# Kernel optimization log

Measured on AMD Instinct MI355X. Metric: run time of the kernel, lower is better.

## Reference

```python
import jax, jax.numpy as jnp
import numpy as np

INF = 1.0e15  # matches the TF module's 1e15 additive mask constant


def setup_inputs() -> dict:
    key = jax.random.key(0)
    kq, kk, kv, kp = jax.random.split(key, 4)
    B, S, D = 8, 4096, 64
    q = jax.random.normal(kq, (B, S, D), dtype=jnp.float32)
    k = jax.random.normal(kk, (B, S, D), dtype=jnp.float32)
    v = jax.random.normal(kv, (B, S, D), dtype=jnp.float32)
    # binary key-padding mask: 1 = masked. Broadcasts over seq_q.
    pad_mask = jax.random.randint(kp, (B, 1, S), 0, 2).astype(jnp.float32)
    # causal look-ahead mask: 1 above the diagonal (future positions masked)
    look_ahead_mask = (1.0 - jnp.tril(jnp.ones((S, S), dtype=jnp.float32)))
    return {"q": q, "k": k, "v": v, "pad_mask": pad_mask,
            "look_ahead_mask": look_ahead_mask}


def reference(q, k, v, pad_mask, look_ahead_mask):
    d_model = jnp.asarray(q.shape[2], dtype=q.dtype)
    # (B, Sq, Sk) score matrix, scaled
    score_logits = jnp.einsum("bqd,bkd->bqk", q, k) / jnp.sqrt(d_model)
    score_logits = score_logits + pad_mask * (-INF)          # broadcast (B,1,Sk)
    score_logits = score_logits + look_ahead_mask * (-INF)   # broadcast (Sq,Sk)
    attention_weight = jax.nn.softmax(score_logits, axis=-1)
    context_vector = jnp.einsum("bqk,bkd->bqd", attention_weight, v)
    return context_vector, attention_weight
```

## Files before the change

kernel.cpp:

```cpp
#include <hip/hip_runtime.h>

#define S_LEN 4096
#define D_DIM 64
#define NEG_BIG 1.0e15f
#define NC1 8
#define SSTAT (8 * 64 * NC1 * 64)
#define NPAD_OFF SSTAT
#define WS_FLOATS_NEEDED (NPAD_OFF + 16)
#define VSTRIDE 70

typedef __bf16 bf16_t;
typedef bf16_t bf16x8 __attribute__((ext_vector_type(8)));
typedef bf16_t bf16x4v __attribute__((ext_vector_type(4)));
typedef bf16_t bf16x2v __attribute__((ext_vector_type(2)));
typedef float f32x4v __attribute__((ext_vector_type(4)));

__global__ __launch_bounds__(256, 2)
void sdpa_stats(const float* __restrict__ Qg,
                const float* __restrict__ Kg,
                const float* __restrict__ Pg,
                float* __restrict__ ws,
                float* __restrict__ ctx)
{
    __shared__ __align__(16) bf16_t Ks[64][72];
    __shared__ float pads[64];

    const int tid  = threadIdx.x;
    const int w    = tid >> 6;
    const int lane = tid & 63;
    const int g    = lane >> 4;
    const int c    = lane & 15;
    const int gx   = blockIdx.x;
    const int b    = gx & 7;
    const int t    = gx >> 3;
    const int qt   = 63 - (t & 63);
    const int kc   = t >> 6;
    const int q0   = qt * 64;

    if (gx >= 2048) {
        f32x4v z = {0.f, 0.f, 0.f, 0.f};
        *(f32x4v*)(ctx + (size_t)(gx - 2048) * 1024 + tid * 4) = z;
    }

    const size_t soff = ((size_t)((b * 64 + qt) * NC1 + kc)) * 64;

    if (kc * 8 > qt) {
        if (tid < 64) ws[soff + tid] = 0.f;
        if (t == 511) {
            float cnt = 0.f, first = (float)S_LEN;
            const float* pb = Pg + (size_t)b * S_LEN;
            for (int i = tid; i < S_LEN; i += 256) {
                float p = pb[i];
                cnt += 1.f - p;
                if (p == 0.f) first = fminf(first, (float)i);
            }
            #pragma unroll
            for (int off = 32; off >= 1; off >>= 1) {
                cnt += __shfl_down(cnt, off);
                first = fminf(first, __shfl_down(first, off));
            }
            if (lane == 0) { pads[w] = cnt; pads[8 + w] = first; }
            __syncthreads();
            if (tid == 0) {
                ws[NPAD_OFF + b]     = pads[0] + pads[1] + pads[2] + pads[3];
                ws[NPAD_OFF + 8 + b] = fminf(fminf(pads[8], pads[9]), fminf(pads[10], pads[11]));
            }
        }
        return;
    }

    bf16x8 qa[2];
    {
        const float* qrow = Qg + ((size_t)b * S_LEN + q0 + 16 * w + c) * D_DIM;
        #pragma unroll
        for (int ks = 0; ks < 2; ++ks) {
            float4 a0 = *(const float4*)(qrow + ks * 32 + 8 * g);
            float4 a1 = *(const float4*)(qrow + ks * 32 + 8 * g + 4);
            qa[ks][0]=(bf16_t)a0.x; qa[ks][1]=(bf16_t)a0.y; qa[ks][2]=(bf16_t)a0.z; qa[ks][3]=(bf16_t)a0.w;
            qa[ks][4]=(bf16_t)a1.x; qa[ks][5]=(bf16_t)a1.y; qa[ks][6]=(bf16_t)a1.z; qa[ks][7]=(bf16_t)a1.w;
        }
    }

    float l[4] = {0.f, 0.f, 0.f, 0.f};
    const int qgBase = q0 + 16 * w + 4 * g;
    const int kend = min(kc * 8 + 8, qt + 1);

    for (int kt = kc * 8; kt < kend; ++kt) {
        const int k0 = kt * 64;
        {
            const float* src = Kg + ((size_t)b * S_LEN + k0) * D_DIM;
            #pragma unroll
            for (int i = 0; i < 4; ++i) {
                int f4 = i * 256 + tid;
                int r  = f4 >> 4;
                int c4 = (f4 & 15) * 4;
                float4 v4 = *(const float4*)(src + (size_t)f4 * 4);
                bf16x4v bv;
                bv[0]=(bf16_t)v4.x; bv[1]=(bf16_t)v4.y; bv[2]=(bf16_t)v4.z; bv[3]=(bf16_t)v4.w;
                *(bf16x4v*)&Ks[r][c4] = bv;
            }
            if (tid < 64) pads[tid] = Pg[(size_t)b * S_LEN + k0 + tid] * (-NEG_BIG);
        }
        __syncthreads();

        f32x4v sc[4];
        #pragma unroll
        for (int ct = 0; ct < 4; ++ct) {
            sc[ct] = (f32x4v){0.f, 0.f, 0.f, 0.f};
            #pragma unroll
            for (int ks = 0; ks < 2; ++ks) {
                bf16x8 kb = *(const bf16x8*)&Ks[ct * 16 + c][ks * 32 + 8 * g];
                sc[ct] = __builtin_amdgcn_mfma_f32_16x16x32_bf16(qa[ks], kb, sc[ct], 0, 0, 0);
            }
        }
        float rs[4] = {0.f, 0.f, 0.f, 0.f};
        #pragma unroll
        for (int ct = 0; ct < 4; ++ct) {
            float pn  = pads[ct * 16 + c];
            int   kgi = k0 + ct * 16 + c;
            #pragma unroll
            for (int r = 0; r < 4; ++r) {
                float lg = sc[ct][r] * 0.125f + pn;
                if (kgi > qgBase + r) lg -= NEG_BIG;
                rs[r] += __expf(lg);
            }
        }
        #pragma unroll
        for (int r = 0; r < 4; ++r) {
            float s = rs[r];
            s += __shfl_xor(s, 1);
            s += __shfl_xor(s, 2);
            s += __shfl_xor(s, 4);
            s += __shfl_xor(s, 8);
            l[r] += s;
        }
        __syncthreads();
    }

    if (c == 0) {
        #pragma unroll
        for (int r = 0; r < 4; ++r)
            ws[soff + 16 * w + 4 * g + r] = l[r];
    }
}

__global__ __launch_bounds__(256, 2)
void sdpa_wpv(const float* __restrict__ Qg,
              const float* __restrict__ Kg,
              const float* __restrict__ Vg,
              const float* __restrict__ Pg,
              float* __restrict__ Wg,
              float* __restrict__ ws,
              float* __restrict__ ctx)
{
    __shared__ __align__(16) bf16_t Ks[64][72];
    __shared__ __align__(16) bf16_t VT[64][VSTRIDE];
    __shared__ __align__(16) bf16_t Pf[64][72];
    __shared__ float pads[64];
    __shared__ float Lrow[64];

    const int tid  = threadIdx.x;
    const int w    = tid >> 6;
    const int lane = tid & 63;
    const int g    = lane >> 4;
    const int c    = lane & 15;
    const int gx   = blockIdx.x;
    const int b    = gx & 7;
    const int t    = gx >> 3;
    const int qt   = 63 - (t & 63);
    const int kc   = t >> 6;
    const int q0   = qt * 64;
    const int kstart = kc * 8;

    const float npadTot = ws[NPAD_OFF + b];
    const float firstNP = ws[NPAD_OFF + 8 + b];
    const bool  blockDeg = ((float)q0 < firstNP);

    if (tid < 64) {
        int qrow = q0 + tid;
        float L;
        if ((float)qrow < firstNP) {
            L = (float)(qrow + 1) + npadTot;
        } else {
            const float* sb = ws + (size_t)(b * 64 + qt) * NC1 * 64 + tid;
            L = 0.f;
            #pragma unroll
            for (int i = 0; i < NC1; ++i) L += sb[(size_t)i * 64];
        }
        Lrow[tid] = 1.f / L;
    }
    __syncthreads();

    float* wchunk = Wg + (size_t)b * S_LEN * S_LEN + (size_t)q0 * S_LEN;

    if (kstart > qt && !blockDeg) {
        const f32x4v z = {0.f, 0.f, 0.f, 0.f};
        for (int kt = kstart; kt < kstart + 8; ++kt) {
            float* wbase = wchunk + kt * 64;
            #pragma unroll
            for (int i = 0; i < 4; ++i) {
                int f4 = i * 256 + tid;
                int r  = f4 >> 4;
                int c4 = (f4 & 15) * 4;
                __builtin_nontemporal_store(z, (f32x4v*)(wbase + (size_t)r * S_LEN + c4));
            }
        }
        return;
    }

    bf16x8 qa[2];
    {
        const float* qrow = Qg + ((size_t)b * S_LEN + q0 + 16 * w + c) * D_DIM;
        #pragma unroll
        for (int ks = 0; ks < 2; ++ks) {
            float4 a0 = *(const float4*)(qrow + ks * 32 + 8 * g);
            float4 a1 = *(const float4*)(qrow + ks * 32 + 8 * g + 4);
            qa[ks][0]=(bf16_t)a0.x; qa[ks][1]=(bf16_t)a0.y; qa[ks][2]=(bf16_t)a0.z; qa[ks][3]=(bf16_t)a0.w;
            qa[ks][4]=(bf16_t)a1.x; qa[ks][5]=(bf16_t)a1.y; qa[ks][6]=(bf16_t)a1.z; qa[ks][7]=(bf16_t)a1.w;
        }
    }

    const int qgBase = q0 + 16 * w + 4 * g;
    float linv[4];
    #pragma unroll
    for (int r = 0; r < 4; ++r) linv[r] = Lrow[16 * w + 4 * g + r];

    f32x4v o[4];
    #pragma unroll
    for (int dt = 0; dt < 4; ++dt) o[dt] = (f32x4v){0.f, 0.f, 0.f, 0.f};

    for (int kt = kstart; kt < kstart + 8; ++kt) {
        const int k0 = kt * 64;
        float* wbase = wchunk + k0;
        const bool cur = (kt <= qt) || blockDeg;

        if (cur) {
            const float* ksrc = Kg + ((size_t)b * S_LEN + k0) * D_DIM;
            const float* vsrc = Vg + ((size_t)b * S_LEN + k0) * D_DIM;
            #pragma unroll
            for (int i = 0; i < 4; ++i) {
                int f4 = i * 256 + tid;
                int r  = f4 >> 4;
                int c4 = (f4 & 15) * 4;
                float4 kv = *(const float4*)(ksrc + (size_t)f4 * 4);
                bf16x4v bv;
                bv[0]=(bf16_t)kv.x; bv[1]=(bf16_t)kv.y; bv[2]=(bf16_t)kv.z; bv[3]=(bf16_t)kv.w;
                *(bf16x4v*)&Ks[r][c4] = bv;
                float4 vv = *(const float4*)(vsrc + (size_t)f4 * 4);
                VT[c4 + 0][r] = (bf16_t)vv.x;
                VT[c4 + 1][r] = (bf16_t)vv.y;
                VT[c4 + 2][r] = (bf16_t)vv.z;
                VT[c4 + 3][r] = (bf16_t)vv.w;
            }
            if (tid < 64) pads[tid] = Pg[(size_t)b * S_LEN + k0 + tid] * (-NEG_BIG);
            __syncthreads();

            f32x4v sc[4];
            #pragma unroll
            for (int ct = 0; ct < 4; ++ct) {
                sc[ct] = (f32x4v){0.f, 0.f, 0.f, 0.f};
                #pragma unroll
                for (int ks = 0; ks < 2; ++ks) {
                    bf16x8 kb = *(const bf16x8*)&Ks[ct * 16 + c][ks * 32 + 8 * g];
                    sc[ct] = __builtin_amdgcn_mfma_f32_16x16x32_bf16(qa[ks], kb, sc[ct], 0, 0, 0);
                }
            }
            if (!blockDeg) {
                #pragma unroll
                for (int ct = 0; ct < 4; ++ct) {
                    float pn  = pads[ct * 16 + c];
                    int   kgi = k0 + ct * 16 + c;
                    #pragma unroll
                    for (int r = 0; r < 4; ++r) {
                        float lg = sc[ct][r] * 0.125f + pn;
                        if (kgi > qgBase + r) lg -= NEG_BIG;
                        float wv = __expf(lg) * linv[r];
                        __builtin_nontemporal_store(wv,
                            wbase + (size_t)(16 * w + 4 * g + r) * S_LEN + ct * 16 + c);
                        Pf[16 * w + 4 * g + r][ct * 16 + c] = (bf16_t)wv;
                    }
                }
            } else {
                #pragma unroll
                for (int ct = 0; ct < 4; ++ct) {
                    float pn  = pads[ct * 16 + c];
                    int   kgi = k0 + ct * 16 + c;
                    #pragma unroll
                    for (int r = 0; r < 4; ++r) {
                        float lg = sc[ct][r] * 0.125f + pn;
                        if (kgi > qgBase + r) lg -= NEG_BIG;
                        float wv = __expf(lg) * linv[r];
                        if ((float)(qgBase + r) < firstNP)
                            wv = (kgi <= qgBase + r || pn == 0.f) ? linv[r] : 0.f;
                        __builtin_nontemporal_store(wv,
                            wbase + (size_t)(16 * w + 4 * g + r) * S_LEN + ct * 16 + c);
                        Pf[16 * w + 4 * g + r][ct * 16 + c] = (bf16_t)wv;
                    }
                }
            }
            __syncthreads();

            #pragma unroll
            for (int ks = 0; ks < 2; ++ks) {
                bf16x8 wa = *(const bf16x8*)&Pf[16 * w + c][ks * 32 + 8 * g];
                #pragma unroll
                for (int dt = 0; dt < 4; ++dt) {
                    bf16x8 vb;
                    #pragma unroll
                    for (int p = 0; p < 4; ++p)
                        ((bf16x2v*)&vb)[p] = *(const bf16x2v*)&VT[dt * 16 + c][ks * 32 + 8 * g + 2 * p];
                    o[dt] = __builtin_amdgcn_mfma_f32_16x16x32_bf16(wa, vb, o[dt], 0, 0, 0);
                }
            }
            __syncthreads();
        } else {
            const f32x4v z = {0.f, 0.f, 0.f, 0.f};
            #pragma unroll
            for (int i = 0; i < 4; ++i) {
                int f4 = i * 256 + tid;
                int r  = f4 >> 4;
                int c4 = (f4 & 15) * 4;
                __builtin_nontemporal_store(z, (f32x4v*)(wbase + (size_t)r * S_LEN + c4));
            }
        }
    }

    #pragma unroll
    for (int dt = 0; dt < 4; ++dt)
        #pragma unroll
        for (int r = 0; r < 4; ++r)
            atomicAdd(&ctx[((size_t)b * S_LEN + (q0 + 16 * w + 4 * g + r)) * D_DIM + dt * 16 + c],
                      o[dt][r]);
}

__global__ __launch_bounds__(256, 2)
void sdpa_fused(const float* __restrict__ Qg,
                const float* __restrict__ Kg,
                const float* __restrict__ Vg,
                const float* __restrict__ Pg,
                float* __restrict__ Og,
                float* __restrict__ Wg)
{
    __shared__ __align__(16) bf16_t Qs[64][72];
    __shared__ __align__(16) bf16_t Ks[64][72];
    __shared__ __align__(16) bf16_t VT[64][72];
    __shared__ __align__(16) float  Wf[64][68];
    __shared__ float pads[64];
    __shared__ float red[4];
    __shared__ int   anyDeg;

    const int tid  = threadIdx.x;
    const int w    = tid >> 6;
    const int lane = tid & 63;
    const int g    = lane >> 4;
    const int c    = lane & 15;
    const int b    = blockIdx.x & 7;
    const int qt   = 63 - (blockIdx.x >> 3);
    const int q0   = qt * 64;

    if (tid == 0) anyDeg = 0;

    {
        const float* src = Qg + ((size_t)b * S_LEN + q0) * D_DIM;
        #pragma unroll
        for (int i = 0; i < 4; ++i) {
            int f4 = i * 256 + tid;
            int r  = f4 >> 4;
            int c4 = (f4 & 15) * 4;
            float4 v4 = *(const float4*)(src + (size_t)f4 * 4);
            bf16x4v bv;
            bv[0]=(bf16_t)v4.x; bv[1]=(bf16_t)v4.y; bv[2]=(bf16_t)v4.z; bv[3]=(bf16_t)v4.w;
            *(bf16x4v*)&Qs[r][c4] = bv;
        }
    }
    __syncthreads();

    bf16x8 qa[2];
    {
        int row = 16 * w + c;
        #pragma unroll
        for (int ks = 0; ks < 2; ++ks)
            qa[ks] = *(const bf16x8*)&Qs[row][ks * 32 + 8 * g];
    }

    float m[4], l[4];
    #pragma unroll
    for (int r = 0; r < 4; ++r) { m[r] = -INFINITY; l[r] = 0.f; }
    const int qgBase = q0 + 16 * w + 4 * g;

    for (int kt = 0; kt <= qt; ++kt) {
        const int k0 = kt * 64;
        {
            const float* src = Kg + ((size_t)b * S_LEN + k0) * D_DIM;
            #pragma unroll
            for (int i = 0; i < 4; ++i) {
                int f4 = i * 256 + tid;
                int r  = f4 >> 4;
                int c4 = (f4 & 15) * 4;
                float4 v4 = *(const float4*)(src + (size_t)f4 * 4);
                bf16x4v bv;
                bv[0]=(bf16_t)v4.x; bv[1]=(bf16_t)v4.y; bv[2]=(bf16_t)v4.z; bv[3]=(bf16_t)v4.w;
                *(bf16x4v*)&Ks[r][c4] = bv;
            }
            if (tid < 64) pads[tid] = Pg[(size_t)b * S_LEN + k0 + tid] * (-NEG_BIG);
        }
        __syncthreads();

        f32x4v sc[4];
        #pragma unroll
        for (int ct = 0; ct < 4; ++ct) {
            sc[ct] = (f32x4v){0.f, 0.f, 0.f, 0.f};
            #pragma unroll
            for (int ks = 0; ks < 2; ++ks) {
                bf16x8 kb = *(const bf16x8*)&Ks[ct * 16 + c][ks * 32 + 8 * g];
                sc[ct] = __builtin_amdgcn_mfma_f32_16x16x32_bf16(qa[ks], kb, sc[ct], 0, 0, 0);
            }
        }
        float l4[4][4];
        #pragma unroll
        for (int ct = 0; ct < 4; ++ct) {
            float pn  = pads[ct * 16 + c];
            int   kgi = k0 + ct * 16 + c;
            #pragma unroll
            for (int r = 0; r < 4; ++r) {
                float lg = sc[ct][r] * 0.125f + pn;
                if (kgi > qgBase + r) lg -= NEG_BIG;
                l4[ct][r] = lg;
            }
        }
        #pragma unroll
        for (int r = 0; r < 4; ++r) {
            float tm = fmaxf(fmaxf(l4[0][r], l4[1][r]), fmaxf(l4[2][r], l4[3][r]));
            tm = fmaxf(tm, __shfl_xor(tm, 1));
            tm = fmaxf(tm, __shfl_xor(tm, 2));
            tm = fmaxf(tm, __shfl_xor(tm, 4));
            tm = fmaxf(tm, __shfl_xor(tm, 8));
            float mnew = fmaxf(m[r], tm);
            float s = __expf(l4[0][r] - mnew) + __expf(l4[1][r] - mnew)
                    + __expf(l4[2][r] - mnew) + __expf(l4[3][r] - mnew);
            s += __shfl_xor(s, 1);
            s += __shfl_xor(s, 2);
            s += __shfl_xor(s, 4);
            s += __shfl_xor(s, 8);
            l[r] = l[r] * __expf(m[r] - mnew) + s;
            m[r] = mnew;
        }
        __syncthreads();
    }

    {
        float cnt = 0.f;
        const float* pb = Pg + (size_t)b * S_LEN;
        for (int i = tid; i < S_LEN; i += 256) cnt += 1.f - pb[i];
        #pragma unroll
        for (int off = 32; off >= 1; off >>= 1) cnt += __shfl_down(cnt, off);
        if (lane == 0) red[w] = cnt;
    }
    __syncthreads();
    {
        float nonpad = red[0] + red[1] + red[2] + red[3];
        bool deg = false;
        #pragma unroll
        for (int r = 0; r < 4; ++r)
            if (m[r] < -1.0e14f) { l[r] += nonpad; deg = true; }
        if (deg) anyDeg = 1;
    }
    __syncthreads();
    const bool blockDeg = (anyDeg != 0);
    float linv[4];
    #pragma unroll
    for (int r = 0; r < 4; ++r) linv[r] = 1.f / l[r];

    f32x4v o[4];
    #pragma unroll
    for (int dt = 0; dt < 4; ++dt) o[dt] = (f32x4v){0.f, 0.f, 0.f, 0.f};

    for (int kt = 0; kt < 64; ++kt) {
        const int k0 = kt * 64;
        float* wbase = Wg + (size_t)b * S_LEN * S_LEN + (size_t)q0 * S_LEN + k0;

        if (kt <= qt || blockDeg) {
            const float* ksrc = Kg + ((size_t)b * S_LEN + k0) * D_DIM;
            const float* vsrc = Vg + ((size_t)b * S_LEN + k0) * D_DIM;
            #pragma unroll
            for (int i = 0; i < 4; ++i) {
                int f4 = i * 256 + tid;
                int r  = f4 >> 4;
                int c4 = (f4 & 15) * 4;
                float4 kv = *(const float4*)(ksrc + (size_t)f4 * 4);
                bf16x4v bv;
                bv[0]=(bf16_t)kv.x; bv[1]=(bf16_t)kv.y; bv[2]=(bf16_t)kv.z; bv[3]=(bf16_t)kv.w;
                *(bf16x4v*)&Ks[r][c4] = bv;
                float4 vv = *(const float4*)(vsrc + (size_t)f4 * 4);
                VT[c4 + 0][r] = (bf16_t)vv.x;
                VT[c4 + 1][r] = (bf16_t)vv.y;
                VT[c4 + 2][r] = (bf16_t)vv.z;
                VT[c4 + 3][r] = (bf16_t)vv.w;
            }
            if (tid < 64) pads[tid] = Pg[(size_t)b * S_LEN + k0 + tid] * (-NEG_BIG);
            __syncthreads();

            f32x4v sc[4];
            #pragma unroll
            for (int ct = 0; ct < 4; ++ct) {
                sc[ct] = (f32x4v){0.f, 0.f, 0.f, 0.f};
                #pragma unroll
                for (int ks = 0; ks < 2; ++ks) {
                    bf16x8 kb = *(const bf16x8*)&Ks[ct * 16 + c][ks * 32 + 8 * g];
                    sc[ct] = __builtin_amdgcn_mfma_f32_16x16x32_bf16(qa[ks], kb, sc[ct], 0, 0, 0);
                }
            }
            #pragma unroll
            for (int ct = 0; ct < 4; ++ct) {
                float pn  = pads[ct * 16 + c];
                int   kgi = k0 + ct * 16 + c;
                #pragma unroll
                for (int r = 0; r < 4; ++r) {
                    float lg = sc[ct][r] * 0.125f + pn;
                    if (kgi > qgBase + r) lg -= NEG_BIG;
                    float wv = __expf(lg - m[r]) * linv[r];
                    Wf[16 * w + 4 * g + r][ct * 16 + c] = wv;
                }
            }
            __syncthreads();

            #pragma unroll
            for (int i = 0; i < 4; ++i) {
                int f4 = i * 256 + tid;
                int r  = f4 >> 4;
                int c4 = (f4 & 15) * 4;
                float4 wv = *(const float4*)&Wf[r][c4];
                *(float4*)(wbase + (size_t)r * S_LEN + c4) = wv;
            }

            #pragma unroll
            for (int ks = 0; ks < 2; ++ks) {
                float4 f0 = *(const float4*)&Wf[16 * w + c][ks * 32 + 8 * g];
                float4 f1 = *(const float4*)&Wf[16 * w + c][ks * 32 + 8 * g + 4];
                bf16x8 wa;
                wa[0]=(bf16_t)f0.x; wa[1]=(bf16_t)f0.y; wa[2]=(bf16_t)f0.z; wa[3]=(bf16_t)f0.w;
                wa[4]=(bf16_t)f1.x; wa[5]=(bf16_t)f1.y; wa[6]=(bf16_t)f1.z; wa[7]=(bf16_t)f1.w;
                #pragma unroll
                for (int dt = 0; dt < 4; ++dt) {
                    bf16x8 vb = *(const bf16x8*)&VT[dt * 16 + c][ks * 32 + 8 * g];
                    o[dt] = __builtin_amdgcn_mfma_f32_16x16x32_bf16(wa, vb, o[dt], 0, 0, 0);
                }
            }
            __syncthreads();
        } else {
            const float4 z = {0.f, 0.f, 0.f, 0.f};
            #pragma unroll
            for (int i = 0; i < 4; ++i) {
                int f4 = i * 256 + tid;
                int r  = f4 >> 4;
                int c4 = (f4 & 15) * 4;
                *(float4*)(wbase + (size_t)r * S_LEN + c4) = z;
            }
        }
    }

    #pragma unroll
    for (int dt = 0; dt < 4; ++dt)
        #pragma unroll
        for (int r = 0; r < 4; ++r)
            Og[((size_t)b * S_LEN + (q0 + 16 * w + 4 * g + r)) * D_DIM + dt * 16 + c] = o[dt][r];
}

extern "C" void kernel_launch(void* const* d_in, const int* in_sizes, int n_in,
                              void* d_out, int out_size, void* d_ws, size_t ws_size,
                              hipStream_t stream) {
    const float* q   = (const float*)d_in[0];
    const float* k   = (const float*)d_in[1];
    const float* v   = (const float*)d_in[2];
    const float* pad = (const float*)d_in[3];

    float* out  = (float*)d_out;
    float* ctx  = out;
    float* attw = out + (size_t)8 * 4096 * 64;
    float* ws   = (float*)d_ws;

    if (ws_size >= (size_t)WS_FLOATS_NEEDED * 4) {
        hipLaunchKernelGGL(sdpa_stats, dim3(4096), dim3(256), 0, stream, q, k, pad, ws, ctx);
        hipLaunchKernelGGL(sdpa_wpv,   dim3(4096), dim3(256), 0, stream, q, k, v, pad, attw, ws, ctx);
    } else {
        hipLaunchKernelGGL(sdpa_fused, dim3(512), dim3(256), 0, stream, q, k, v, pad, ctx, attw);
    }
}
```

Measured before the change: 192.6 us.

## Merge stats and weight kernels into one ticket-ordered launch with flag dependencies

```diff
diff --git a/kernel.cpp b/kernel.cpp
--- a/kernel.cpp
+++ b/kernel.cpp
@@ -6,7 +6,9 @@
 #define NC1 8
 #define SSTAT (8 * 64 * NC1 * 64)
 #define NPAD_OFF SSTAT
-#define WS_FLOATS_NEEDED (NPAD_OFF + 16)
+#define FLAGS_OFF (NPAD_OFF + 16)
+#define TICKET_OFF (FLAGS_OFF + 512)
+#define WS_FLOATS_NEEDED (TICKET_OFF + 1)
 #define VSTRIDE 70
 
 typedef __bf16 bf16_t;
@@ -15,166 +17,200 @@
 typedef bf16_t bf16x2v __attribute__((ext_vector_type(2)));
 typedef float f32x4v __attribute__((ext_vector_type(4)));
 
+__global__ void sdpa_prep(const float* __restrict__ Pg, float* __restrict__ ws)
+{
+    __shared__ float red[16];
+    const int b   = blockIdx.x;
+    const int tid = threadIdx.x;
+    int* flags = (int*)(ws + FLAGS_OFF);
+    if (tid < 64) flags[b * 64 + tid] = 0;
+    if (b == 0 && tid == 128) ((int*)(ws + TICKET_OFF))[0] = 0;
+
+    float cnt = 0.f, first = (float)S_LEN;
+    const float* pb = Pg + (size_t)b * S_LEN;
+    for (int i = tid; i < S_LEN; i += 256) {
+        float p = pb[i];
+        cnt += 1.f - p;
+        if (p == 0.f) first = fminf(first, (float)i);
+    }
+    #pragma unroll
+    for (int off = 32; off >= 1; off >>= 1) {
+        cnt += __shfl_down(cnt, off);
+        first = fminf(first, __shfl_down(first, off));
+    }
+    const int w = tid >> 6, lane = tid & 63;
+    if (lane == 0) { red[w] = cnt; red[8 + w] = first; }
+    __syncthreads();
+    if (tid == 0) {
+        ws[NPAD_OFF + b]     = red[0] + red[1] + red[2] + red[3];
+        ws[NPAD_OFF + 8 + b] = fminf(fminf(red[8], red[9]), fminf(red[10], red[11]));
+    }
+}
+
 __global__ __launch_bounds__(256, 2)
-void sdpa_stats(const float* __restrict__ Qg,
-                const float* __restrict__ Kg,
-                const float* __restrict__ Pg,
-                float* __restrict__ ws,
-                float* __restrict__ ctx)
-{
-    __shared__ __align__(16) bf16_t Ks[64][72];
-    __shared__ float pads[64];
-
-    const int tid  = threadIdx.x;
-    const int w    = tid >> 6;
-    const int lane = tid & 63;
-    const int g    = lane >> 4;
-    const int c    = lane & 15;
-    const int gx   = blockIdx.x;
-    const int b    = gx & 7;
-    const int t    = gx >> 3;
-    const int qt   = 63 - (t & 63);
-    const int kc   = t >> 6;
-    const int q0   = qt * 64;
-
-    if (gx >= 2048) {
-        f32x4v z = {0.f, 0.f, 0.f, 0.f};
-        *(f32x4v*)(ctx + (size_t)(gx - 2048) * 1024 + tid * 4) = z;
-    }
-
-    const size_t soff = ((size_t)((b * 64 + qt) * NC1 + kc)) * 64;
-
-    if (kc * 8 > qt) {
-        if (tid < 64) ws[soff + tid] = 0.f;
-        if (t == 511) {
-            float cnt = 0.f, first = (float)S_LEN;
-            const float* pb = Pg + (size_t)b * S_LEN;
-            for (int i = tid; i < S_LEN; i += 256) {
-                float p = pb[i];
-                cnt += 1.f - p;
-                if (p == 0.f) first = fminf(first, (float)i);
-            }
-            #pragma unroll
-            for (int off = 32; off >= 1; off >>= 1) {
-                cnt += __shfl_down(cnt, off);
-                first = fminf(first, __shfl_down(first, off));
-            }
-            if (lane == 0) { pads[w] = cnt; pads[8 + w] = first; }
-            __syncthreads();
-            if (tid == 0) {
-                ws[NPAD_OFF + b]     = pads[0] + pads[1] + pads[2] + pads[3];
-                ws[NPAD_OFF + 8 + b] = fminf(fminf(pads[8], pads[9]), fminf(pads[10], pads[11]));
-            }
-        }
-        return;
-    }
-
-    bf16x8 qa[2];
-    {
-        const float* qrow = Qg + ((size_t)b * S_LEN + q0 + 16 * w + c) * D_DIM;
-        #pragma unroll
-        for (int ks = 0; ks < 2; ++ks) {
-            float4 a0 = *(const float4*)(qrow + ks * 32 + 8 * g);
-            float4 a1 = *(const float4*)(qrow + ks * 32 + 8 * g + 4);
-            qa[ks][0]=(bf16_t)a0.x; qa[ks][1]=(bf16_t)a0.y; qa[ks][2]=(bf16_t)a0.z; qa[ks][3]=(bf16_t)a0.w;
-            qa[ks][4]=(bf16_t)a1.x; qa[ks][5]=(bf16_t)a1.y; qa[ks][6]=(bf16_t)a1.z; qa[ks][7]=(bf16_t)a1.w;
-        }
-    }
-
-    float l[4] = {0.f, 0.f, 0.f, 0.f};
-    const int qgBase = q0 + 16 * w + 4 * g;
-    const int kend = min(kc * 8 + 8, qt + 1);
-
-    for (int kt = kc * 8; kt < kend; ++kt) {
-        const int k0 = kt * 64;
-        {
-            const float* src = Kg + ((size_t)b * S_LEN + k0) * D_DIM;
-            #pragma unroll
-            for (int i = 0; i < 4; ++i) {
-                int f4 = i * 256 + tid;
-                int r  = f4 >> 4;
-                int c4 = (f4 & 15) * 4;
-                float4 v4 = *(const float4*)(src + (size_t)f4 * 4);
-                bf16x4v bv;
-                bv[0]=(bf16_t)v4.x; bv[1]=(bf16_t)v4.y; bv[2]=(bf16_t)v4.z; bv[3]=(bf16_t)v4.w;
-                *(bf16x4v*)&Ks[r][c4] = bv;
-            }
-            if (tid < 64) pads[tid] = Pg[(size_t)b * S_LEN + k0 + tid] * (-NEG_BIG);
-        }
-        __syncthreads();
-
-        f32x4v sc[4];
-        #pragma unroll
-        for (int ct = 0; ct < 4; ++ct) {
-            sc[ct] = (f32x4v){0.f, 0.f, 0.f, 0.f};
-            #pragma unroll
-            for (int ks = 0; ks < 2; ++ks) {
-                bf16x8 kb = *(const bf16x8*)&Ks[ct * 16 + c][ks * 32 + 8 * g];
-                sc[ct] = __builtin_amdgcn_mfma_f32_16x16x32_bf16(qa[ks], kb, sc[ct], 0, 0, 0);
-            }
-        }
-        float rs[4] = {0.f, 0.f, 0.f, 0.f};
-        #pragma unroll
-        for (int ct = 0; ct < 4; ++ct) {
-            float pn  = pads[ct * 16 + c];
-            int   kgi = k0 + ct * 16 + c;
-            #pragma unroll
-            for (int r = 0; r < 4; ++r) {
-                float lg = sc[ct][r] * 0.125f + pn;
-                if (kgi > qgBase + r) lg -= NEG_BIG;
-                rs[r] += __expf(lg);
-            }
-        }
-        #pragma unroll
-        for (int r = 0; r < 4; ++r) {
-            float s = rs[r];
-            s += __shfl_xor(s, 1);
-            s += __shfl_xor(s, 2);
-            s += __shfl_xor(s, 4);
-            s += __shfl_xor(s, 8);
-            l[r] += s;
-        }
-        __syncthreads();
-    }
-
-    if (c == 0) {
-        #pragma unroll
-        for (int r = 0; r < 4; ++r)
-            ws[soff + 16 * w + 4 * g + r] = l[r];
-    }
-}
-
-__global__ __launch_bounds__(256, 2)
-void sdpa_wpv(const float* __restrict__ Qg,
-              const float* __restrict__ Kg,
-              const float* __restrict__ Vg,
-              const float* __restrict__ Pg,
-              float* __restrict__ Wg,
-              float* __restrict__ ws,
-              float* __restrict__ ctx)
+void sdpa_main(const float* __restrict__ Qg,
+               const float* __restrict__ Kg,
+               const float* __restrict__ Vg,
+               const float* __restrict__ Pg,
+               float* __restrict__ Wg,
+               float* __restrict__ ws,
+               float* __restrict__ ctx)
 {
     __shared__ __align__(16) bf16_t Ks[64][72];
     __shared__ __align__(16) bf16_t VT[64][VSTRIDE];
     __shared__ __align__(16) bf16_t Pf[64][72];
     __shared__ float pads[64];
     __shared__ float Lrow[64];
-
-    const int tid  = threadIdx.x;
+    __shared__ int   tkt;
+
+    const int tid = threadIdx.x;
+    int* flags = (int*)(ws + FLAGS_OFF);
+    if (tid == 0) tkt = atomicAdd((int*)(ws + TICKET_OFF), 1);
+    __syncthreads();
+    const int ticket = tkt;
+
     const int w    = tid >> 6;
     const int lane = tid & 63;
     const int g    = lane >> 4;
     const int c    = lane & 15;
-    const int gx   = blockIdx.x;
-    const int b    = gx & 7;
-    const int t    = gx >> 3;
-    const int qt   = 63 - (t & 63);
-    const int kc   = t >> 6;
-    const int q0   = qt * 64;
+
+    if (ticket < 4096) {
+        const int qt  = 63 - (ticket >> 6);
+        const int rem = ticket & 63;
+        const int kc  = rem >> 3;
+        const int b   = rem & 7;
+        const int q0  = qt * 64;
+        const int bqt = b * 64 + qt;
+
+        if (kc > (qt >> 3)) {
+            if (tid == 0) { __threadfence(); atomicAdd(flags + bqt, 1); }
+            return;
+        }
+
+        if (kc == 0) {
+            f32x4v z = {0.f, 0.f, 0.f, 0.f};
+            float* cb = ctx + ((size_t)b * S_LEN + q0) * D_DIM;
+            #pragma unroll
+            for (int i = 0; i < 4; ++i)
+                *(f32x4v*)(cb + i * 1024 + tid * 4) = z;
+        }
+
+        bf16x8 qa[2];
+        {
+            const float* qrow = Qg + ((size_t)b * S_LEN + q0 + 16 * w + c) * D_DIM;
+            #pragma unroll
+            for (int ks = 0; ks < 2; ++ks) {
+                float4 a0 = *(const float4*)(qrow + ks * 32 + 8 * g);
+                float4 a1 = *(const float4*)(qrow + ks * 32 + 8 * g + 4);
+                qa[ks][0]=(bf16_t)a0.x; qa[ks][1]=(bf16_t)a0.y; qa[ks][2]=(bf16_t)a0.z; qa[ks][3]=(bf16_t)a0.w;
+                qa[ks][4]=(bf16_t)a1.x; qa[ks][5]=(bf16_t)a1.y; qa[ks][6]=(bf16_t)a1.z; qa[ks][7]=(bf16_t)a1.w;
+            }
+        }
+
+        float l[4] = {0.f, 0.f, 0.f, 0.f};
+        const int qgBase = q0 + 16 * w + 4 * g;
+        const int kend = min(kc * 8 + 8, qt + 1);
+
+        for (int kt = kc * 8; kt < kend; ++kt) {
+            const int k0 = kt * 64;
+            {
+                const float* src = Kg + ((size_t)b * S_LEN + k0) * D_DIM;
+                #pragma unroll
+                for (int i = 0; i < 4; ++i) {
+                    int f4 = i * 256 + tid;
+                    int r  = f4 >> 4;
+                    int c4 = (f4 & 15) * 4;
+                    float4 v4 = *(const float4*)(src + (size_t)f4 * 4);
+                    bf16x4v bv;
+                    bv[0]=(bf16_t)v4.x; bv[1]=(bf16_t)v4.y; bv[2]=(bf16_t)v4.z; bv[3]=(bf16_t)v4.w;
+                    *(bf16x4v*)&Ks[r][c4] = bv;
+                }
+                if (tid < 64) pads[tid] = Pg[(size_t)b * S_LEN + k0 + tid] * (-NEG_BIG);
+            }
+            __syncthreads();
+
+            f32x4v sc[4];
+            #pragma unroll
+            for (int ct = 0; ct < 4; ++ct) {
+                sc[ct] = (f32x4v){0.f, 0.f, 0.f, 0.f};
+                #pragma unroll
+                for (int ks = 0; ks < 2; ++ks) {
+                    bf16x8 kb = *(const bf16x8*)&Ks[ct * 16 + c][ks * 32 + 8 * g];
+                    sc[ct] = __builtin_amdgcn_mfma_f32_16x16x32_bf16(qa[ks], kb, sc[ct], 0, 0, 0);
+                }
+            }
+            float rs[4] = {0.f, 0.f, 0.f, 0.f};
+            #pragma unroll
+            for (int ct = 0; ct < 4; ++ct) {
+                float pn  = pads[ct * 16 + c];
+                int   kgi = k0 + ct * 16 + c;
+                #pragma unroll
+                for (int r = 0; r < 4; ++r) {
+                    float lg = sc[ct][r] * 0.125f + pn;
+                    if (kgi > qgBase + r) lg -= NEG_BIG;
+                    rs[r] += __expf(lg);
+                }
+            }
+            #pragma unroll
+            for (int r = 0; r < 4; ++r) {
+                float s = rs[r];
+                s += __shfl_xor(s, 1);
+                s += __shfl_xor(s, 2);
+                s += __shfl_xor(s, 4);
+                s += __shfl_xor(s, 8);
+                l[r] += s;
+            }
+            __syncthreads();
+        }
+
+        const size_t soff = ((size_t)(bqt * NC1 + kc)) * 64;
+        if (c == 0) {
+            #pragma unroll
+            for (int r = 0; r < 4; ++r)
+                ws[soff + 16 * w + 4 * g + r] = l[r];
+        }
+        __syncthreads();
+        if (tid == 0) { __threadfence(); atomicAdd(flags + bqt, 1); }
+        return;
+    }
+
+    const int jt  = ticket - 4096;
+    const int qt  = 63 - (jt >> 6);
+    const int rem = jt & 63;
+    const int kc  = rem >> 3;
+    const int b   = rem & 7;
+    const int q0  = qt * 64;
     const int kstart = kc * 8;
+    const int bqt = b * 64 + qt;
 
     const float npadTot = ws[NPAD_OFF + b];
     const float firstNP = ws[NPAD_OFF + 8 + b];
     const bool  blockDeg = ((float)q0 < firstNP);
+
+    float* wchunk = Wg + (size_t)b * S_LEN * S_LEN + (size_t)q0 * S_LEN;
+
+    if (kstart > qt && !blockDeg) {
+        const f32x4v z = {0.f, 0.f, 0.f, 0.f};
+        for (int kt = kstart; kt < kstart + 8; ++kt) {
+            float* wbase = wchunk + kt * 64;
+            #pragma unroll
+            for (int i = 0; i < 4; ++i) {
+                int f4 = i * 256 + tid;
+                int r  = f4 >> 4;
+                int c4 = (f4 & 15) * 4;
+                __builtin_nontemporal_store(z, (f32x4v*)(wbase + (size_t)r * S_LEN + c4));
+            }
+        }
+        return;
+    }
+
+    if (tid == 0) {
+        int* fl = flags + bqt;
+        while (__hip_atomic_load(fl, __ATOMIC_ACQUIRE, __HIP_MEMORY_SCOPE_AGENT) != 8)
+            __builtin_amdgcn_s_sleep(2);
+    }
+    __syncthreads();
+    __threadfence();
 
     if (tid < 64) {
         int qrow = q0 + tid;
@@ -182,31 +218,14 @@
         if ((float)qrow < firstNP) {
             L = (float)(qrow + 1) + npadTot;
         } else {
-            const float* sb = ws + (size_t)(b * 64 + qt) * NC1 * 64 + tid;
+            const float* sb = ws + (size_t)bqt * NC1 * 64 + tid;
             L = 0.f;
-            #pragma unroll
-            for (int i = 0; i < NC1; ++i) L += sb[(size_t)i * 64];
+            const int need = (qt >> 3) + 1;
+            for (int i = 0; i < need; ++i) L += sb[(size_t)i * 64];
         }
         Lrow[tid] = 1.f / L;
     }
     __syncthreads();
-
-    float* wchunk = Wg + (size_t)b * S_LEN * S_LEN + (size_t)q0 * S_LEN;
-
-    if (kstart > qt && !blockDeg) {
-        const f32x4v z = {0.f, 0.f, 0.f, 0.f};
-        for (int kt = kstart; kt < kstart + 8; ++kt) {
-            float* wbase = wchunk + kt * 64;
-            #pragma unroll
-            for (int i = 0; i < 4; ++i) {
-                int f4 = i * 256 + tid;
-                int r  = f4 >> 4;
-                int c4 = (f4 & 15) * 4;
-                __builtin_nontemporal_store(z, (f32x4v*)(wbase + (size_t)r * S_LEN + c4));
-            }
-        }
-        return;
-    }
 
     bf16x8 qa[2];
     {
@@ -580,8 +599,9 @@
     float* ws   = (float*)d_ws;
 
     if (ws_size >= (size_t)WS_FLOATS_NEEDED * 4) {
-        hipLaunchKernelGGL(sdpa_stats, dim3(4096), dim3(256), 0, stream, q, k, pad, ws, ctx);
-        hipLaunchKernelGGL(sdpa_wpv,   dim3(4096), dim3(256), 0, stream, q, k, v, pad, attw, ws, ctx);
+        hipLaunchKernelGGL(sdpa_prep, dim3(8), dim3(256), 0, stream, pad, ws);
+        hipLaunchKernelGGL(sdpa_main, dim3(8192), dim3(256), 0, stream,
+                           q, k, v, pad, attw, ws, ctx);
     } else {
         hipLaunchKernelGGL(sdpa_fused, dim3(512), dim3(256), 0, stream, q, k, v, pad, ctx, attw);
     }
```

New measurement: 636.0 us. 230% more time.
